# Performance work log

Measured on AMD Instinct MI355X. Metric: run time of the kernel, lower is better.

Reference implementation:

```python
import jax, jax.numpy as jnp
import numpy as np

CAPACITY = 0.75      # MoDRouter capacity
ACT_STEPS = 3        # act_max_steps
EPS = 0.01           # ACT halting epsilon
PONDER = 0.01        # act_ponder_cost


def setup_inputs() -> dict:
    key = jax.random.key(0)
    k1, k2, k3 = jax.random.split(key, 3)
    x = jax.random.normal(k1, (4, 8192, 1024), dtype=jnp.float32)
    router_w = jax.random.normal(k2, (1024,), dtype=jnp.float32) * 0.02  # nn.Linear(dim,1,bias=False), std=0.02
    halt_w = jax.random.normal(k3, (1024,), dtype=jnp.float32) * 0.02    # halt linear weight (zeros-init in src; perturbed for nontrivial signal)
    halt_b = -jnp.ones((1,), dtype=jnp.float32)                          # halt bias init -1.0
    return {"x": x, "router_w": router_w, "halt_w": halt_w, "halt_b": halt_b}


def _mod_step(x, router_w):
    """MoDRouter.forward + identity block + MoDRouter.scatter_back."""
    b, s, d = x.shape
    k = max(1, int(s * CAPACITY))
    scores = jnp.einsum('bsd,d->bs', x, router_w)                 # (b, s)
    topk_scores, idx = jax.lax.top_k(scores, k)                   # sorted desc, like torch.topk
    routed = jnp.take_along_axis(x, idx[:, :, None], axis=1)      # (b, k, d) gather
    processed = routed                                            # identity stand-in for Block (undefined in source)
    w = jax.nn.softmax(topk_scores, axis=1)[:, :, None]           # straight-through weights (b, k, 1)
    new_vals = processed * w + (1.0 - w) * routed                 # weighted_processed + (1-w)*original_at_indices
    return x.at[jnp.arange(b)[:, None], idx].set(new_vals)        # scatter back; unrouted tokens = identity


def _act_combine(states, halt_w, halt_b):
    """ACTHaltingUnit.forward: masked accumulation over recurrence steps."""
    b, s, d = states[0].shape
    dt = states[0].dtype
    acc = jnp.zeros((b, s), dt)
    out = jnp.zeros((b, s, d), dt)
    rem = jnp.ones((b, s), dt)
    n_upd = jnp.zeros((b, s), dt)
    for state in states:  # fixed small loop over recurrence steps
        h = jax.nn.sigmoid(jnp.einsum('bsd,d->bs', state, halt_w) + halt_b[0])
        still = (acc < 1.0 - EPS).astype(dt)
        new_acc = acc + h * still
        use_rem = (new_acc > 1.0 - EPS).astype(dt) * still
        use_h = (1.0 - use_rem) * still
        p = use_h * h + use_rem * rem
        out = out + p[:, :, None] * state
        acc = acc + p * still
        rem = rem - p * still
        n_upd = n_upd + still
    ponder_loss = PONDER * jnp.mean(n_upd)
    return out, ponder_loss


def reference(x, router_w, halt_w, halt_b):
    states = []
    cur = x
    for _ in range(ACT_STEPS):
        cur = _mod_step(cur, router_w)
        states.append(cur)
    return _act_combine(states, halt_w, halt_b)
```

## Files before the change

### kernel.cpp

```cpp
#include <hip/hip_runtime.h>
#include <math.h>

#define N_TOKENS 32768
#define DIM      1024
#define N_SLOTS  64
#define SLOT_STRIDE 32

typedef float v4f __attribute__((ext_vector_type(4)));

__global__ void modgpt_init(int* __restrict__ n_acc) {
    if (blockIdx.x == 0 && threadIdx.x < N_SLOTS)
        n_acc[threadIdx.x * SLOT_STRIDE] = 0;
}

__global__ __launch_bounds__(256) void modgpt_main(
        const float* __restrict__ x,
        const float* __restrict__ halt_w,
        const float* __restrict__ halt_b,
        float* __restrict__ out,
        int* __restrict__ n_acc) {
    const int wave = threadIdx.x >> 6;
    const int lane = threadIdx.x & 63;
    const int token = blockIdx.x * 4 + wave;

    const v4f* __restrict__ xin = (const v4f*)(x + (size_t)token * DIM);
    v4f* __restrict__ op        = (v4f*)(out + (size_t)token * DIM);
    const v4f* __restrict__ w4  = (const v4f*)halt_w;

    const v4f c0 = xin[lane];
    const v4f c1 = xin[lane + 64];
    const v4f c2 = xin[lane + 128];
    const v4f c3 = xin[lane + 192];

    const v4f w0 = w4[lane];
    const v4f w1 = w4[lane + 64];
    const v4f w2 = w4[lane + 128];
    const v4f w3 = w4[lane + 192];
    const float hb = halt_b[0];

    v4f m = c0 * w0 + c1 * w1 + c2 * w2 + c3 * w3;
    float dot = m.x + m.y + m.z + m.w;
    #pragma unroll
    for (int off = 32; off >= 1; off >>= 1)
        dot += __shfl_xor(dot, off, 64);

    const float h = 1.0f / (1.0f + expf(-(dot + hb)));

    float acc = 0.0f, rem = 1.0f, P = 0.0f;
    int n = 0;
    #pragma unroll
    for (int s = 0; s < 3; ++s) {
        if (acc < 0.99f) {
            const float na = acc + h;
            const float p  = (na > 0.99f) ? rem : h;
            P   += p;
            acc += p;
            rem -= p;
            n   += 1;
        }
    }

    op[lane]       = c0 * P;
    op[lane + 64]  = c1 * P;
    op[lane + 128] = c2 * P;
    op[lane + 192] = c3 * P;

    __shared__ int sn[4];
    if (lane == 0) sn[wave] = n;
    __syncthreads();
    if (threadIdx.x == 0)
        atomicAdd(n_acc + (blockIdx.x & (N_SLOTS - 1)) * SLOT_STRIDE,
                  sn[0] + sn[1] + sn[2] + sn[3]);
}

__global__ void modgpt_finalize(const int* __restrict__ n_acc,
                                float* __restrict__ ponder_out) {
    int v = n_acc[(threadIdx.x & 63) * SLOT_STRIDE];
    #pragma unroll
    for (int off = 32; off >= 1; off >>= 1)
        v += __shfl_xor(v, off, 64);
    if (threadIdx.x == 0)
        ponder_out[0] = 0.01f * ((float)v / (float)N_TOKENS);
}

extern "C" void kernel_launch(void* const* d_in, const int* in_sizes, int n_in,
                              void* d_out, int out_size, void* d_ws, size_t ws_size,
                              hipStream_t stream) {
    const float* x        = (const float*)d_in[0];
    const float* halt_w   = (const float*)d_in[2];
    const float* halt_b   = (const float*)d_in[3];
    float* out            = (float*)d_out;
    int*   n_acc          = (int*)d_ws;

    modgpt_init<<<1, 64, 0, stream>>>(n_acc);
    modgpt_main<<<N_TOKENS / 4, 256, 0, stream>>>(x, halt_w, halt_b, out, n_acc);
    modgpt_finalize<<<1, 64, 0, stream>>>(n_acc, out + (size_t)N_TOKENS * DIM);
}
```

Baseline: 235.7 us.

## Split halting computation into separate dot and scale kernels

Splits the fused kernel in two. The first computes the halting dot product for two tokens per wave and stores the per-token ACT weight P in a workspace buffer. The second rereads x and writes the scaled output, processing four tokens per wave with software prefetch of the next token. The aim is better memory-level parallelism in each phase, at the cost of reading x a second time and an extra kernel launch.

```diff
diff --git a/kernel.cpp b/kernel.cpp
--- a/kernel.cpp
+++ b/kernel.cpp
@@ -13,39 +13,7 @@
         n_acc[threadIdx.x * SLOT_STRIDE] = 0;
 }
 
-__global__ __launch_bounds__(256) void modgpt_main(
-        const float* __restrict__ x,
-        const float* __restrict__ halt_w,
-        const float* __restrict__ halt_b,
-        float* __restrict__ out,
-        int* __restrict__ n_acc) {
-    const int wave = threadIdx.x >> 6;
-    const int lane = threadIdx.x & 63;
-    const int token = blockIdx.x * 4 + wave;
-
-    const v4f* __restrict__ xin = (const v4f*)(x + (size_t)token * DIM);
-    v4f* __restrict__ op        = (v4f*)(out + (size_t)token * DIM);
-    const v4f* __restrict__ w4  = (const v4f*)halt_w;
-
-    const v4f c0 = xin[lane];
-    const v4f c1 = xin[lane + 64];
-    const v4f c2 = xin[lane + 128];
-    const v4f c3 = xin[lane + 192];
-
-    const v4f w0 = w4[lane];
-    const v4f w1 = w4[lane + 64];
-    const v4f w2 = w4[lane + 128];
-    const v4f w3 = w4[lane + 192];
-    const float hb = halt_b[0];
-
-    v4f m = c0 * w0 + c1 * w1 + c2 * w2 + c3 * w3;
-    float dot = m.x + m.y + m.z + m.w;
-    #pragma unroll
-    for (int off = 32; off >= 1; off >>= 1)
-        dot += __shfl_xor(dot, off, 64);
-
-    const float h = 1.0f / (1.0f + expf(-(dot + hb)));
-
+__device__ __forceinline__ void act_recur(float h, float* P_out, int* n_out) {
     float acc = 0.0f, rem = 1.0f, P = 0.0f;
     int n = 0;
     #pragma unroll
@@ -59,18 +27,109 @@
             n   += 1;
         }
     }
+    *P_out = P;
+    *n_out = n;
+}
 
-    op[lane]       = c0 * P;
-    op[lane + 64]  = c1 * P;
-    op[lane + 128] = c2 * P;
-    op[lane + 192] = c3 * P;
+__global__ __launch_bounds__(256) void modgpt_dot(
+        const float* __restrict__ x,
+        const float* __restrict__ halt_w,
+        const float* __restrict__ halt_b,
+        float* __restrict__ Pbuf,
+        int* __restrict__ n_acc) {
+    const int wave = threadIdx.x >> 6;
+    const int lane = threadIdx.x & 63;
+    const int tok0 = (blockIdx.x * 4 + wave) * 2;
+
+    const v4f* __restrict__ xin = (const v4f*)(x + (size_t)tok0 * DIM);
+    const v4f* __restrict__ w4  = (const v4f*)halt_w;
+
+    const v4f a0 = xin[lane];
+    const v4f a1 = xin[lane + 64];
+    const v4f a2 = xin[lane + 128];
+    const v4f a3 = xin[lane + 192];
+    const v4f b0 = xin[lane + 256];
+    const v4f b1 = xin[lane + 320];
+    const v4f b2 = xin[lane + 384];
+    const v4f b3 = xin[lane + 448];
+
+    const v4f w0 = w4[lane];
+    const v4f w1 = w4[lane + 64];
+    const v4f w2 = w4[lane + 128];
+    const v4f w3 = w4[lane + 192];
+    const float hb = halt_b[0];
+
+    float P0, P1;
+    int n0, n1;
+    {
+        v4f m = a0 * w0 + a1 * w1 + a2 * w2 + a3 * w3;
+        float dot = m.x + m.y + m.z + m.w;
+        #pragma unroll
+        for (int off = 32; off >= 1; off >>= 1)
+            dot += __shfl_xor(dot, off, 64);
+        act_recur(1.0f / (1.0f + expf(-(dot + hb))), &P0, &n0);
+    }
+    {
+        v4f m = b0 * w0 + b1 * w1 + b2 * w2 + b3 * w3;
+        float dot = m.x + m.y + m.z + m.w;
+        #pragma unroll
+        for (int off = 32; off >= 1; off >>= 1)
+            dot += __shfl_xor(dot, off, 64);
+        act_recur(1.0f / (1.0f + expf(-(dot + hb))), &P1, &n1);
+    }
+
+    if (lane == 0) {
+        Pbuf[tok0]     = P0;
+        Pbuf[tok0 + 1] = P1;
+    }
 
     __shared__ int sn[4];
-    if (lane == 0) sn[wave] = n;
+    if (lane == 0) sn[wave] = n0 + n1;
     __syncthreads();
     if (threadIdx.x == 0)
         atomicAdd(n_acc + (blockIdx.x & (N_SLOTS - 1)) * SLOT_STRIDE,
                   sn[0] + sn[1] + sn[2] + sn[3]);
+}
+
+#define SCALE_BLOCKS 2048
+#define TOK_PER_WAVE2 4
+
+__global__ __launch_bounds__(256) void modgpt_scale(
+        const float* __restrict__ x,
+        const float* __restrict__ Pbuf,
+        float* __restrict__ out) {
+    const int wave = threadIdx.x >> 6;
+    const int lane = threadIdx.x & 63;
+    const int tok0 = (blockIdx.x * 4 + wave) * TOK_PER_WAVE2;
+
+    const v4f* __restrict__ xi = (const v4f*)(x + (size_t)tok0 * DIM);
+    v4f* __restrict__ op       = (v4f*)(out + (size_t)tok0 * DIM);
+
+    v4f c0 = xi[lane];
+    v4f c1 = xi[lane + 64];
+    v4f c2 = xi[lane + 128];
+    v4f c3 = xi[lane + 192];
+    float P = Pbuf[tok0];
+
+    #pragma unroll
+    for (int t = 0; t < TOK_PER_WAVE2; ++t) {
+        v4f p0, p1, p2, p3;
+        float Pn;
+        if (t + 1 < TOK_PER_WAVE2) {
+            const v4f* nx = xi + (size_t)(t + 1) * 256;
+            p0 = nx[lane];
+            p1 = nx[lane + 64];
+            p2 = nx[lane + 128];
+            p3 = nx[lane + 192];
+            Pn = Pbuf[tok0 + t + 1];
+        }
+        v4f* o = op + (size_t)t * 256;
+        o[lane]       = c0 * P;
+        o[lane + 64]  = c1 * P;
+        o[lane + 128] = c2 * P;
+        o[lane + 192] = c3 * P;
+        c0 = p0; c1 = p1; c2 = p2; c3 = p3; P = Pn;
+    }
 }
 
 __global__ void modgpt_finalize(const int* __restrict__ n_acc,
@@ -91,8 +150,10 @@
     const float* halt_b   = (const float*)d_in[3];
     float* out            = (float*)d_out;
     int*   n_acc          = (int*)d_ws;
+    float* Pbuf           = (float*)((char*)d_ws + 8192);
 
     modgpt_init<<<1, 64, 0, stream>>>(n_acc);
-    modgpt_main<<<N_TOKENS / 4, 256, 0, stream>>>(x, halt_w, halt_b, out, n_acc);
+    modgpt_dot<<<N_TOKENS / 8, 256, 0, stream>>>(x, halt_w, halt_b, Pbuf, n_acc);
+    modgpt_scale<<<SCALE_BLOCKS, 256, 0, stream>>>(x, Pbuf, out);
     modgpt_finalize<<<1, 64, 0, stream>>>(n_acc, out + (size_t)N_TOKENS * DIM);
 }
```

Measured after the change: 257.7 us. +9.3%, slower.
